# Performance work log

Measured on AMD Instinct MI355X. Metric: run time of the kernel, lower is better.

Reference implementation:

```python
import jax, jax.numpy as jnp
import numpy as np

N, E, D, H, L = 50000, 800000, 256, 256, 4
EMB = 2 * H  # OGB format: MLP hidden width
BN_EPS = 1e-5


def _bn(h, gamma, beta):
    # training-mode BatchNorm1d: biased batch stats over node dim
    m = jnp.mean(h, axis=0)
    v = jnp.mean((h - m) ** 2, axis=0)
    return gamma * (h - m) / jnp.sqrt(v + BN_EPS) + beta


def setup_inputs() -> dict:
    key = jax.random.key(0)
    ks = jax.random.split(key, 12)
    x = jax.random.normal(ks[0], (N, D), dtype=jnp.float32)
    edge_index = jax.random.randint(ks[1], (2, E), 0, N, dtype=jnp.int64)
    s1 = 1.0 / np.sqrt(D)
    s2 = 1.0 / np.sqrt(EMB)
    return {
        "x": x,
        "edge_index": edge_index,
        "W1": jax.random.uniform(ks[2], (L, D, EMB), jnp.float32, -s1, s1),
        "b1": jax.random.uniform(ks[3], (L, EMB), jnp.float32, -s1, s1),
        "bn1_gamma": jnp.ones((L, EMB), jnp.float32),
        "bn1_beta": jnp.zeros((L, EMB), jnp.float32),
        "W2": jax.random.uniform(ks[4], (L, EMB, H), jnp.float32, -s2, s2),
        "b2": jax.random.uniform(ks[5], (L, H), jnp.float32, -s2, s2),
        "bn2_gamma": jnp.ones((L, H), jnp.float32),
        "bn2_beta": jnp.zeros((L, H), jnp.float32),
    }


def reference(x, edge_index, W1, b1, bn1_gamma, bn1_beta, W2, b2, bn2_gamma, bn2_beta):
    src, dst = edge_index[0], edge_index[1]
    n = x.shape[0]
    h = x
    for l in range(L):
        # GINConv with eps=0: (1+eps)*h_i + sum_{j->i} h_j
        agg = h + jax.ops.segment_sum(h[src], dst, num_segments=n)
        # inner MLP: Linear -> BN -> ReLU -> Linear
        z = jax.nn.relu(_bn(agg @ W1[l] + b1[l], bn1_gamma[l], bn1_beta[l]))
        z = z @ W2[l] + b2[l]
        # outer BN; ReLU except last layer (dropout = identity in eval/reference)
        z = _bn(z, bn2_gamma[l], bn2_beta[l])
        h = z if l == L - 1 else jax.nn.relu(z)
    return h
```

## Files before the change

### kernel.cpp

```cpp
#include <hip/hip_runtime.h>
#include <stdint.h>

#define NN 50000
#define NE 800000
#define DD 256
#define EM 512
#define NL 4
#define EPS 1e-5f

typedef unsigned short u16;
typedef __attribute__((ext_vector_type(4))) unsigned short u16x4;
typedef __attribute__((ext_vector_type(8))) short s16x8;
typedef __attribute__((ext_vector_type(8))) float f32x8;
typedef __attribute__((ext_vector_type(4))) float f32x4;
typedef __attribute__((ext_vector_type(8))) __bf16 bf16x8;

union Frag { s16x8 s; bf16x8 b; };

__device__ __forceinline__ float bf2f(u16 h) {
  unsigned u = ((unsigned)h) << 16;
  return __builtin_bit_cast(float, u);
}
__device__ __forceinline__ u16 f2bf(float f) {
  unsigned u = __builtin_bit_cast(unsigned, f);
  u = (u + 0x7FFFu + ((u >> 16) & 1u)) >> 16;
  return (u16)u;
}
__device__ __forceinline__ void bfsplit(float f, u16& hi, u16& lo) {
  hi = f2bf(f);
  lo = f2bf(f - bf2f(hi));
}

__device__ __forceinline__ void gload16(const u16* g, u16* l) {
  __builtin_amdgcn_global_load_lds(
      (const __attribute__((address_space(1))) unsigned int*)g,
      (__attribute__((address_space(3))) unsigned int*)l, 16, 0, 0);
}


__global__ void k_f32_to_bf16(const float* __restrict__ in, u16* __restrict__ out, int n8) {
  int i = blockIdx.x * blockDim.x + threadIdx.x;
  int stride = gridDim.x * blockDim.x;
  for (; i < n8; i += stride) {
    f32x8 v = ((const f32x8*)in)[i];
    s16x8 o;
#pragma unroll
    for (int j = 0; j < 8; j++) o[j] = (short)f2bf(v[j]);
    ((s16x8*)out)[i] = o;
  }
}

__global__ void k_prep_w(const float* __restrict__ W, u16* __restrict__ WThi,
                         u16* __restrict__ WTlo, int K, int Nc) {
  int total = NL * K * Nc;
  for (int i = blockIdx.x * blockDim.x + threadIdx.x; i < total; i += gridDim.x * blockDim.x) {
    int l = i / (K * Nc);
    int rem = i - l * (K * Nc);
    int k = rem / Nc;
    int n = rem - k * Nc;
    float v = W[i];
    u16 hi, lo; bfsplit(v, hi, lo);
    size_t o = (size_t)l * Nc * K + (size_t)n * K + k;
    WThi[o] = hi; WTlo[o] = lo;
  }
}

__global__ void k_deg(const int* __restrict__ dst, int* __restrict__ deg) {
  for (int e = blockIdx.x * blockDim.x + threadIdx.x; e < NE; e += gridDim.x * blockDim.x)
    atomicAdd(&deg[dst[e]], 1);
}

#define SCB 49

__global__ __launch_bounds__(1024) void k_scan1(const int* __restrict__ deg,
                                                int* __restrict__ rowptr,
                                                int* __restrict__ part) {
  __shared__ int sm[1024];
  int t = threadIdx.x, b = blockIdx.x;
  int idx = b * 1024 + t;
  int v = (idx < NN) ? deg[idx] : 0;
  sm[t] = v;
  __syncthreads();
  for (int off = 1; off < 1024; off <<= 1) {
    int u = (t >= off) ? sm[t - off] : 0;
    __syncthreads();
    sm[t] += u;
    __syncthreads();
  }
  int incl = sm[t];
  if (idx < NN) rowptr[idx] = incl - v;
  if (t == 1023) part[b] = incl;
}

__global__ void k_scan2(int* __restrict__ part, int* __restrict__ rowptr) {
  int t = threadIdx.x;
  int v = (t < SCB) ? part[t] : 0;
  int orig = v;
  for (int off = 1; off < 64; off <<= 1) {
    int u = __shfl_up(v, off);
    if (t >= off) v += u;
  }
  if (t < SCB) part[t] = v - orig;
  if (t == SCB - 1) rowptr[NN] = v;
}

__global__ __launch_bounds__(1024) void k_scan3(int* __restrict__ rowptr,
                                                const int* __restrict__ part) {
  int idx = blockIdx.x * 1024 + threadIdx.x;
  if (idx < NN) rowptr[idx] += part[blockIdx.x];
}

__global__ void k_fill(const int* __restrict__ src, const int* __restrict__ dst,
                       const int* __restrict__ rowptr, int* __restrict__ cursor,
                       int* __restrict__ cols) {
  for (int e = blockIdx.x * blockDim.x + threadIdx.x; e < NE; e += gridDim.x * blockDim.x) {
    int d = dst[e];
    int pos = atomicAdd(&cursor[d], 1);
    cols[rowptr[d] + pos] = src[e];
  }
}


template <bool FUSED>
__global__ __launch_bounds__(256) void k_agg(const u16* __restrict__ src,
                                             const float* __restrict__ ss,
                                             const int* __restrict__ rowptr,
                                             const int* __restrict__ cols,
                                             u16* __restrict__ Ahi,
                                             u16* __restrict__ Alo) {
  int wid = threadIdx.x >> 6, lane = threadIdx.x & 63;
  int node = blockIdx.x * 4 + wid;
  int c0 = lane << 2;
  f32x4 sc, sh;
  if (FUSED) {
    sc = *(const f32x4*)(ss + c0);
    sh = *(const f32x4*)(ss + DD + c0);
  }
  u16x4 v = *(const u16x4*)(src + (size_t)node * DD + c0);
  f32x4 a;
#pragma unroll
  for (int j = 0; j < 4; j++) {
    float f = bf2f(v[j]);
    a[j] = FUSED ? fmaxf(f * sc[j] + sh[j], 0.f) : f;
  }
  int beg = rowptr[node], end = rowptr[node + 1];
  int e = beg;
  for (; e + 3 < end; e += 4) {
    int s0 = cols[e], s1 = cols[e + 1], s2 = cols[e + 2], s3 = cols[e + 3];
    u16x4 w0 = *(const u16x4*)(src + (size_t)s0 * DD + c0);
    u16x4 w1 = *(const u16x4*)(src + (size_t)s1 * DD + c0);
    u16x4 w2 = *(const u16x4*)(src + (size_t)s2 * DD + c0);
    u16x4 w3 = *(const u16x4*)(src + (size_t)s3 * DD + c0);
#pragma unroll
    for (int j = 0; j < 4; j++) {
      float f0 = bf2f(w0[j]), f1 = bf2f(w1[j]), f2 = bf2f(w2[j]), f3 = bf2f(w3[j]);
      if (FUSED) {
        f0 = fmaxf(f0 * sc[j] + sh[j], 0.f);
        f1 = fmaxf(f1 * sc[j] + sh[j], 0.f);
        f2 = fmaxf(f2 * sc[j] + sh[j], 0.f);
        f3 = fmaxf(f3 * sc[j] + sh[j], 0.f);
      }
      a[j] += f0; a[j] += f1; a[j] += f2; a[j] += f3;
    }
  }
  for (; e < end; ++e) {
    int s = cols[e];
    u16x4 w = *(const u16x4*)(src + (size_t)s * DD + c0);
#pragma unroll
    for (int j = 0; j < 4; j++) {
      float f = bf2f(w[j]);
      a[j] += FUSED ? fmaxf(f * sc[j] + sh[j], 0.f) : f;
    }
  }
  u16x4 oh, ol;
#pragma unroll
  for (int j = 0; j < 4; j++) { u16 hi, lo; bfsplit(a[j], hi, lo); oh[j] = hi; ol[j] = lo; }
  *(u16x4*)(Ahi + (size_t)node * DD + c0) = oh;
  *(u16x4*)(Alo + (size_t)node * DD + c0) = ol;
}

template <int K, int NC, bool OUT_BF16, int NSEG>
__global__ __launch_bounds__(256) void k_gemm(const u16* __restrict__ Ahi,
                                              const u16* __restrict__ Alo,
                                              const u16* __restrict__ WThi,
                                              const u16* __restrict__ WTlo,
                                              const float* __restrict__ bias,
                                              void* __restrict__ Zout,
                                              float* __restrict__ stats, int M) {
  constexpr int NCB = NC / 128;
  int nxb = (M + 127) >> 7;
  int bid = blockIdx.x;
  int slot = bid & 7;
  int ycb  = (bid >> 3) & (NCB - 1);
  int grp  = bid / (8 * NCB);
  int xb   = grp * 8 + slot;
  if (xb >= nxb) return;
  int brow = xb * 128;
  int bcol = ycb * 128;

  __shared__ u16 AlHi[128 * 32];
  __shared__ u16 AlLo[NSEG == 3 ? 128 * 32 : 64];
  __shared__ u16 BlHi[128 * 32];
  __shared__ u16 BlLo[128 * 32];
  __shared__ float sblk[256];
  int tid = threadIdx.x;
  sblk[tid] = 0.f;
  int lane = tid & 63, wid = tid >> 6;
  int wm = wid & 1, wn = wid >> 1;

  f32x4 zero = {0.f, 0.f, 0.f, 0.f};
  f32x4 acc[4][4];
#pragma unroll
  for (int m = 0; m < 4; m++)
#pragma unroll
    for (int n = 0; n < 4; n++) acc[m][n] = zero;

  int rinc = lane >> 2;
  int cq = (lane & 3) * 8;
  long ra0 = brow + wid * 16 + rinc;  if (ra0 > M - 1) ra0 = M - 1;
  long ra1 = brow + 64 + wid * 16 + rinc; if (ra1 > M - 1) ra1 = M - 1;
  long rb0 = bcol + wid * 16 + rinc;
  long rb1 = bcol + 64 + wid * 16 + rinc;

  const u16* gAh0 = Ahi + ra0 * K + cq;
  const u16* gAh1 = Ahi + ra1 * K + cq;
  const u16* gAl0 = Alo + ra0 * K + cq;
  const u16* gAl1 = Alo + ra1 * K + cq;
  const u16* gBh0 = WThi + rb0 * K + cq;
  const u16* gBh1 = WThi + rb1 * K + cq;
  const u16* gBl0 = WTlo + rb0 * K + cq;
  const u16* gBl1 = WTlo + rb1 * K + cq;
  int lc0 = wid * 512, lc1 = (wid + 4) * 512;

  int fr = lane & 15;
  int kk = (lane >> 4) * 8;
  int fo = (wm * 64 + fr) * 32 + kk;
  int go = (wn * 64 + fr) * 32 + kk;

  const int KS = K / 32;
  for (int kt = 0; kt < KS; ++kt) {
    int k0 = kt * 32;
    gload16(gAh0 + k0, &AlHi[lc0]);
    gload16(gAh1 + k0, &AlHi[lc1]);
    if (NSEG == 3) {
      gload16(gAl0 + k0, &AlLo[lc0]);
      gload16(gAl1 + k0, &AlLo[lc1]);
    }
    gload16(gBh0 + k0, &BlHi[lc0]);
    gload16(gBh1 + k0, &BlHi[lc1]);
    gload16(gBl0 + k0, &BlLo[lc0]);
    gload16(gBl1 + k0, &BlLo[lc1]);
    __syncthreads();

    Frag aH[4], bH[4], bL[4];
#pragma unroll
    for (int m = 0; m < 4; m++) aH[m].s = *(const s16x8*)(&AlHi[fo + m * 512]);
#pragma unroll
    for (int n = 0; n < 4; n++) bH[n].s = *(const s16x8*)(&BlHi[go + n * 512]);
#pragma unroll
    for (int n = 0; n < 4; n++) bL[n].s = *(const s16x8*)(&BlLo[go + n * 512]);
#pragma unroll
    for (int m = 0; m < 4; m++)
#pragma unroll
      for (int n = 0; n < 4; n++)
        acc[m][n] = __builtin_amdgcn_mfma_f32_16x16x32_bf16(aH[m].b, bH[n].b, acc[m][n], 0, 0, 0);
    if (NSEG == 3) {
      Frag aL[4];
#pragma unroll
      for (int m = 0; m < 4; m++) aL[m].s = *(const s16x8*)(&AlLo[fo + m * 512]);
#pragma unroll
      for (int m = 0; m < 4; m++)
#pragma unroll
        for (int n = 0; n < 4; n++)
          acc[m][n] = __builtin_amdgcn_mfma_f32_16x16x32_bf16(aL[m].b, bH[n].b, acc[m][n], 0, 0, 0);
    }
#pragma unroll
    for (int m = 0; m < 4; m++)
#pragma unroll
      for (int n = 0; n < 4; n++)
        acc[m][n] = __builtin_amdgcn_mfma_f32_16x16x32_bf16(aH[m].b, bL[n].b, acc[m][n], 0, 0, 0);
    __syncthreads();
  }

  int colb = bcol + wn * 64;
  float bv[4];
#pragma unroll
  for (int n = 0; n < 4; n++) bv[n] = bias[colb + n * 16 + fr];
  int rb = brow + wm * 64 + ((lane >> 4) << 2);
  float sn[4] = {0.f, 0.f, 0.f, 0.f}, qn[4] = {0.f, 0.f, 0.f, 0.f};
#pragma unroll
  for (int m = 0; m < 4; m++) {
#pragma unroll
    for (int r = 0; r < 4; r++) {
      int row = rb + m * 16 + r;
      if (row < M) {
        size_t base = (size_t)row * NC + colb + fr;
#pragma unroll
        for (int n = 0; n < 4; n++) {
          float z = acc[m][n][r] + bv[n];
          if (OUT_BF16) ((u16*)Zout)[base + n * 16] = f2bf(z);
          else          ((float*)Zout)[base + n * 16] = z;
          sn[n] += z; qn[n] += z * z;
        }
      }
    }
  }
#pragma unroll
  for (int n = 0; n < 4; n++) {
    sn[n] += __shfl_xor(sn[n], 16); sn[n] += __shfl_xor(sn[n], 32);
    qn[n] += __shfl_xor(qn[n], 16); qn[n] += __shfl_xor(qn[n], 32);
  }
  if (lane < 16) {
#pragma unroll
    for (int n = 0; n < 4; n++) {
      atomicAdd(&sblk[wn * 64 + n * 16 + lane], sn[n]);
      atomicAdd(&sblk[128 + wn * 64 + n * 16 + lane], qn[n]);
    }
  }
  __syncthreads();
  if (tid < 128) atomicAdd(&stats[bcol + tid], sblk[tid]);
  else           atomicAdd(&stats[NC + bcol + (tid - 128)], sblk[tid]);
}

__global__ void k_finalize(const float* __restrict__ stats, const float* __restrict__ gamma,
                           const float* __restrict__ beta, float* __restrict__ ss, int NC) {
  int c = blockIdx.x * blockDim.x + threadIdx.x;
  if (c < NC) {
    float mean = stats[c] * (1.0f / NN);
    float var = stats[NC + c] * (1.0f / NN) - mean * mean;
    float sc = gamma[c] * rsqrtf(var + EPS);
    ss[c] = sc;
    ss[NC + c] = beta[c] - mean * sc;
  }
}

template <int NC>
__global__ void k_bn_a2(const u16* __restrict__ Z, const float* __restrict__ ss,
                        u16* __restrict__ A2, int n8) {
  int i = blockIdx.x * blockDim.x + threadIdx.x;
  int stride = gridDim.x * blockDim.x;
  for (; i < n8; i += stride) {
    int c = (i * 8) & (NC - 1);
    s16x8 v = *(const s16x8*)(Z + (size_t)i * 8);
    s16x8 o;
#pragma unroll
    for (int j = 0; j < 8; j++) {
      float f = fmaxf(bf2f((u16)v[j]) * ss[c + j] + ss[NC + c + j], 0.f);
      o[j] = (short)f2bf(f);
    }
    *(s16x8*)(A2 + (size_t)i * 8) = o;
  }
}

template <int NC>
__global__ void k_bn_out(const float* __restrict__ Z, const float* __restrict__ ss,
                         float* __restrict__ out, int n4) {
  int i = blockIdx.x * blockDim.x + threadIdx.x;
  int stride = gridDim.x * blockDim.x;
  for (; i < n4; i += stride) {
    int c = (i * 4) & (NC - 1);
    f32x4 v = *(const f32x4*)(Z + (size_t)i * 4);
    f32x4 o;
#pragma unroll
    for (int j = 0; j < 4; j++) o[j] = v[j] * ss[c + j] + ss[NC + c + j];
    *(f32x4*)(out + (size_t)i * 4) = o;
  }
}


extern "C" void kernel_launch(void* const* d_in, const int* in_sizes, int n_in,
                              void* d_out, int out_size, void* d_ws, size_t ws_size,
                              hipStream_t stream) {
  const float* x  = (const float*)d_in[0];
  const int* ei   = (const int*)d_in[1];
  const int* esrc = ei;
  const int* edst = ei + NE;
  const float* W1 = (const float*)d_in[2];
  const float* b1 = (const float*)d_in[3];
  const float* g1 = (const float*)d_in[4];
  const float* be1= (const float*)d_in[5];
  const float* W2 = (const float*)d_in[6];
  const float* b2 = (const float*)d_in[7];
  const float* g2 = (const float*)d_in[8];
  const float* be2= (const float*)d_in[9];
  float* out = (float*)d_out;

  char* w = (char*)d_ws;
  auto alloc = [&](size_t bytes) {
    char* p = w;
    w += (bytes + 255) & ~(size_t)255;
    return p;
  };
  char* R0 = alloc((size_t)NN * EM * 2);
  char* R1 = alloc((size_t)NN * EM * 2);
  u16* W1hi = (u16*)alloc((size_t)NL * EM * DD * 2);
  u16* W1lo = (u16*)alloc((size_t)NL * EM * DD * 2);
  u16* W2hi = (u16*)alloc((size_t)NL * DD * EM * 2);
  u16* W2lo = (u16*)alloc((size_t)NL * DD * EM * 2);
  char* zbase = (char*)alloc((size_t)NN * 4);
  int* deg    = (int*)zbase;
  int* cursor = (int*)alloc((size_t)NN * 4);
  float* stats1 = (float*)alloc((size_t)NL * 2 * EM * 4);
  float* stats2 = (float*)alloc((size_t)NL * 2 * DD * 4);
  size_t zspan = (char*)w - zbase;
  int* rowptr = (int*)alloc((size_t)(NN + 1) * 4);
  int* part   = (int*)alloc(64 * 4);
  int* cols   = (int*)alloc((size_t)NE * 4);
  float* ss1  = (float*)alloc(2 * EM * 4);
  float* ss2  = (float*)alloc(2 * DD * 4);

  u16*   Hb   = (u16*)R0;
  u16*   Z1   = (u16*)R0;
  float* Z2f  = (float*)R0;
  u16*   A1hi = (u16*)R1;
  u16*   A1lo = (u16*)R1 + (size_t)NN * DD;
  u16*   A2   = (u16*)R1;

  hipMemsetAsync(zbase, 0, zspan, stream);
  k_deg<<<2048, 256, 0, stream>>>(edst, deg);
  k_scan1<<<SCB, 1024, 0, stream>>>(deg, rowptr, part);
  k_scan2<<<1, 64, 0, stream>>>(part, rowptr);
  k_scan3<<<SCB, 1024, 0, stream>>>(rowptr, part);
  k_fill<<<2048, 256, 0, stream>>>(esrc, edst, rowptr, cursor, cols);
  k_prep_w<<<2048, 256, 0, stream>>>(W1, W1hi, W1lo, DD, EM);
  k_prep_w<<<2048, 256, 0, stream>>>(W2, W2hi, W2lo, EM, DD);
  k_f32_to_bf16<<<2048, 256, 0, stream>>>(x, Hb, NN * DD / 8);

  const int NXB = (NN + 127) / 128;
  const int G1GRID = ((NXB + 7) / 8) * 8 * (EM / 128);
  const int G2GRID = ((NXB + 7) / 8) * 8 * (DD / 128);

  for (int l = 0; l < NL; ++l) {
    float* st1 = stats1 + (size_t)l * 2 * EM;
    float* st2 = stats2 + (size_t)l * 2 * DD;
    if (l == 0)
      k_agg<false><<<NN / 4, 256, 0, stream>>>(Hb, nullptr, rowptr, cols, A1hi, A1lo);
    else
      k_agg<true><<<NN / 4, 256, 0, stream>>>(Hb, ss2, rowptr, cols, A1hi, A1lo);

    k_gemm<DD, EM, true, 3><<<G1GRID, 256, 0, stream>>>(
        A1hi, A1lo, W1hi + (size_t)l * EM * DD, W1lo + (size_t)l * EM * DD,
        b1 + (size_t)l * EM, Z1, st1, NN);
    k_finalize<<<2, 256, 0, stream>>>(st1, g1 + (size_t)l * EM, be1 + (size_t)l * EM, ss1, EM);
    k_bn_a2<EM><<<2048, 256, 0, stream>>>(Z1, ss1, A2, NN * EM / 8);

    if (l < NL - 1) {
      k_gemm<EM, DD, true, 2><<<G2GRID, 256, 0, stream>>>(
          A2, A2, W2hi + (size_t)l * DD * EM, W2lo + (size_t)l * DD * EM,
          b2 + (size_t)l * DD, Hb, st2, NN);
    } else {
      k_gemm<EM, DD, false, 2><<<G2GRID, 256, 0, stream>>>(
          A2, A2, W2hi + (size_t)l * DD * EM, W2lo + (size_t)l * DD * EM,
          b2 + (size_t)l * DD, Z2f, st2, NN);
    }
    k_finalize<<<1, 256, 0, stream>>>(st2, g2 + (size_t)l * DD, be2 + (size_t)l * DD, ss2, DD);
  }
  k_bn_out<DD><<<2048, 256, 0, stream>>>(Z2f, ss2, out, NN * DD / 4);
}
```

Before: 980.3 us.

## Fuse BN1+ReLU into second GEMM A-load and fold finalize into consumers

The BN1 normalize+ReLU pass (k_bn_a2) is removed. GEMM2 now reads the bf16 Z1 directly into registers, applies scale/shift/ReLU computed in shared memory from the raw stats, and writes the result to LDS as the A tile. The k_finalize kernels are eliminated by computing scale/shift inline in k_agg, k_gemm2 and k_bn_out. The last layer's output becomes bf16 instead of fp32, which saves a full pass over a 50Kx512 tensor plus several launches, but it trades the async global-to-LDS loads for register staging in GEMM2 and changes the final layer's precision.

```diff
diff --git a/kernel.cpp b/kernel.cpp
--- a/kernel.cpp
+++ b/kernel.cpp
@@ -7,6 +7,7 @@
 #define EM 512
 #define NL 4
 #define EPS 1e-5f
+#define RN (1.0f / NN)
 
 typedef unsigned short u16;
 typedef __attribute__((ext_vector_type(4))) unsigned short u16x4;
@@ -123,7 +124,9 @@
 
 template <bool FUSED>
 __global__ __launch_bounds__(256) void k_agg(const u16* __restrict__ src,
-                                             const float* __restrict__ ss,
+                                             const float* __restrict__ st,
+                                             const float* __restrict__ ga,
+                                             const float* __restrict__ be,
                                              const int* __restrict__ rowptr,
                                              const int* __restrict__ cols,
                                              u16* __restrict__ Ahi,
@@ -133,8 +136,17 @@
   int c0 = lane << 2;
   f32x4 sc, sh;
   if (FUSED) {
-    sc = *(const f32x4*)(ss + c0);
-    sh = *(const f32x4*)(ss + DD + c0);
+    f32x4 m = *(const f32x4*)(st + c0);
+    f32x4 q = *(const f32x4*)(st + DD + c0);
+    f32x4 g = *(const f32x4*)(ga + c0);
+    f32x4 b = *(const f32x4*)(be + c0);
+#pragma unroll
+    for (int j = 0; j < 4; j++) {
+      float mean = m[j] * RN;
+      float var = q[j] * RN - mean * mean;
+      sc[j] = g[j] * rsqrtf(var + EPS);
+      sh[j] = b[j] - mean * sc[j];
+    }
   }
   u16x4 v = *(const u16x4*)(src + (size_t)node * DD + c0);
   f32x4 a;
@@ -179,14 +191,14 @@
   *(u16x4*)(Alo + (size_t)node * DD + c0) = ol;
 }
 
-template <int K, int NC, bool OUT_BF16, int NSEG>
-__global__ __launch_bounds__(256) void k_gemm(const u16* __restrict__ Ahi,
-                                              const u16* __restrict__ Alo,
-                                              const u16* __restrict__ WThi,
-                                              const u16* __restrict__ WTlo,
-                                              const float* __restrict__ bias,
-                                              void* __restrict__ Zout,
-                                              float* __restrict__ stats, int M) {
+template <int K, int NC>
+__global__ __launch_bounds__(256) void k_gemm1(const u16* __restrict__ Ahi,
+                                               const u16* __restrict__ Alo,
+                                               const u16* __restrict__ WThi,
+                                               const u16* __restrict__ WTlo,
+                                               const float* __restrict__ bias,
+                                               u16* __restrict__ Zout,
+                                               float* __restrict__ stats, int M) {
   constexpr int NCB = NC / 128;
   int nxb = (M + 127) >> 7;
   int bid = blockIdx.x;
@@ -199,7 +211,7 @@
   int bcol = ycb * 128;
 
   __shared__ u16 AlHi[128 * 32];
-  __shared__ u16 AlLo[NSEG == 3 ? 128 * 32 : 64];
+  __shared__ u16 AlLo[128 * 32];
   __shared__ u16 BlHi[128 * 32];
   __shared__ u16 BlLo[128 * 32];
   __shared__ float sblk[256];
@@ -242,17 +254,15 @@
     int k0 = kt * 32;
     gload16(gAh0 + k0, &AlHi[lc0]);
     gload16(gAh1 + k0, &AlHi[lc1]);
-    if (NSEG == 3) {
-      gload16(gAl0 + k0, &AlLo[lc0]);
-      gload16(gAl1 + k0, &AlLo[lc1]);
-    }
+    gload16(gAl0 + k0, &AlLo[lc0]);
+    gload16(gAl1 + k0, &AlLo[lc1]);
     gload16(gBh0 + k0, &BlHi[lc0]);
     gload16(gBh1 + k0, &BlHi[lc1]);
     gload16(gBl0 + k0, &BlLo[lc0]);
     gload16(gBl1 + k0, &BlLo[lc1]);
     __syncthreads();
 
-    Frag aH[4], bH[4], bL[4];
+    Frag aH[4], bH[4], bL[4], aL[4];
 #pragma unroll
     for (int m = 0; m < 4; m++) aH[m].s = *(const s16x8*)(&AlHi[fo + m * 512]);
 #pragma unroll
@@ -264,16 +274,13 @@
 #pragma unroll
       for (int n = 0; n < 4; n++)
         acc[m][n] = __builtin_amdgcn_mfma_f32_16x16x32_bf16(aH[m].b, bH[n].b, acc[m][n], 0, 0, 0);
-    if (NSEG == 3) {
-      Frag aL[4];
-#pragma unroll
-      for (int m = 0; m < 4; m++) aL[m].s = *(const s16x8*)(&AlLo[fo + m * 512]);
-#pragma unroll
-      for (int m = 0; m < 4; m++)
-#pragma unroll
-        for (int n = 0; n < 4; n++)
-          acc[m][n] = __builtin_amdgcn_mfma_f32_16x16x32_bf16(aL[m].b, bH[n].b, acc[m][n], 0, 0, 0);
-    }
+#pragma unroll
+    for (int m = 0; m < 4; m++) aL[m].s = *(const s16x8*)(&AlLo[fo + m * 512]);
+#pragma unroll
+    for (int m = 0; m < 4; m++)
+#pragma unroll
+      for (int n = 0; n < 4; n++)
+        acc[m][n] = __builtin_amdgcn_mfma_f32_16x16x32_bf16(aL[m].b, bH[n].b, acc[m][n], 0, 0, 0);
 #pragma unroll
     for (int m = 0; m < 4; m++)
 #pragma unroll
@@ -298,8 +305,7 @@
 #pragma unroll
         for (int n = 0; n < 4; n++) {
           float z = acc[m][n][r] + bv[n];
-          if (OUT_BF16) ((u16*)Zout)[base + n * 16] = f2bf(z);
-          else          ((float*)Zout)[base + n * 16] = z;
+          Zout[base + n * 16] = f2bf(z);
           sn[n] += z; qn[n] += z * z;
         }
       }
@@ -322,47 +328,178 @@
   else           atomicAdd(&stats[NC + bcol + (tid - 128)], sblk[tid]);
 }
 
-__global__ void k_finalize(const float* __restrict__ stats, const float* __restrict__ gamma,
-                           const float* __restrict__ beta, float* __restrict__ ss, int NC) {
-  int c = blockIdx.x * blockDim.x + threadIdx.x;
-  if (c < NC) {
-    float mean = stats[c] * (1.0f / NN);
-    float var = stats[NC + c] * (1.0f / NN) - mean * mean;
-    float sc = gamma[c] * rsqrtf(var + EPS);
-    ss[c] = sc;
-    ss[NC + c] = beta[c] - mean * sc;
-  }
-}
-
-template <int NC>
-__global__ void k_bn_a2(const u16* __restrict__ Z, const float* __restrict__ ss,
-                        u16* __restrict__ A2, int n8) {
-  int i = blockIdx.x * blockDim.x + threadIdx.x;
-  int stride = gridDim.x * blockDim.x;
-  for (; i < n8; i += stride) {
-    int c = (i * 8) & (NC - 1);
-    s16x8 v = *(const s16x8*)(Z + (size_t)i * 8);
-    s16x8 o;
-#pragma unroll
-    for (int j = 0; j < 8; j++) {
-      float f = fmaxf(bf2f((u16)v[j]) * ss[c + j] + ss[NC + c + j], 0.f);
-      o[j] = (short)f2bf(f);
-    }
-    *(s16x8*)(A2 + (size_t)i * 8) = o;
-  }
-}
-
-template <int NC>
-__global__ void k_bn_out(const float* __restrict__ Z, const float* __restrict__ ss,
+__global__ __launch_bounds__(256) void k_gemm2(const u16* __restrict__ Z1,
+                                               const u16* __restrict__ WThi,
+                                               const u16* __restrict__ WTlo,
+                                               const float* __restrict__ bias,
+                                               const float* __restrict__ st1,
+                                               const float* __restrict__ g1,
+                                               const float* __restrict__ be1,
+                                               u16* __restrict__ Hout,
+                                               float* __restrict__ stats, int M) {
+  constexpr int K = EM, NC = DD, NCB = NC / 128;
+  int nxb = (M + 127) >> 7;
+  int bid = blockIdx.x;
+  int slot = bid & 7;
+  int ycb  = (bid >> 3) & (NCB - 1);
+  int grp  = bid / (8 * NCB);
+  int xb   = grp * 8 + slot;
+  if (xb >= nxb) return;
+  int brow = xb * 128;
+  int bcol = ycb * 128;
+
+  __shared__ u16 AlHi[128 * 32];
+  __shared__ u16 BlHi[128 * 32];
+  __shared__ u16 BlLo[128 * 32];
+  __shared__ float scL[EM];
+  __shared__ float shL[EM];
+  __shared__ float sblk[256];
+  int tid = threadIdx.x;
+  sblk[tid] = 0.f;
+  for (int c = tid; c < EM; c += 256) {
+    float mean = st1[c] * RN;
+    float var = st1[EM + c] * RN - mean * mean;
+    float s = g1[c] * rsqrtf(var + EPS);
+    scL[c] = s;
+    shL[c] = be1[c] - mean * s;
+  }
+  int lane = tid & 63, wid = tid >> 6;
+  int wm = wid & 1, wn = wid >> 1;
+
+  f32x4 zero = {0.f, 0.f, 0.f, 0.f};
+  f32x4 acc[4][4];
+#pragma unroll
+  for (int m = 0; m < 4; m++)
+#pragma unroll
+    for (int n = 0; n < 4; n++) acc[m][n] = zero;
+
+  int rinc = lane >> 2;
+  int cq = (lane & 3) * 8;
+  long ra0 = brow + wid * 16 + rinc;  if (ra0 > M - 1) ra0 = M - 1;
+  long ra1 = brow + 64 + wid * 16 + rinc; if (ra1 > M - 1) ra1 = M - 1;
+  long rb0 = bcol + wid * 16 + rinc;
+  long rb1 = bcol + 64 + wid * 16 + rinc;
+
+  const u16* gZ0 = Z1 + ra0 * K + cq;
+  const u16* gZ1 = Z1 + ra1 * K + cq;
+  const u16* gBh0 = WThi + rb0 * K + cq;
+  const u16* gBh1 = WThi + rb1 * K + cq;
+  const u16* gBl0 = WTlo + rb0 * K + cq;
+  const u16* gBl1 = WTlo + rb1 * K + cq;
+  int lc0 = wid * 512, lc1 = (wid + 4) * 512;
+
+  int fr = lane & 15;
+  int kk = (lane >> 4) * 8;
+  int fo = (wm * 64 + fr) * 32 + kk;
+  int go = (wn * 64 + fr) * 32 + kk;
+
+  __syncthreads();
+
+  const int KS = K / 32;
+  for (int kt = 0; kt < KS; ++kt) {
+    int k0 = kt * 32;
+    s16x8 z0 = *(const s16x8*)(gZ0 + k0);
+    s16x8 z1 = *(const s16x8*)(gZ1 + k0);
+    gload16(gBh0 + k0, &BlHi[lc0]);
+    gload16(gBh1 + k0, &BlHi[lc1]);
+    gload16(gBl0 + k0, &BlLo[lc0]);
+    gload16(gBl1 + k0, &BlLo[lc1]);
+    f32x4 s0 = *(const f32x4*)(&scL[k0 + cq]);
+    f32x4 s1 = *(const f32x4*)(&scL[k0 + cq + 4]);
+    f32x4 h0 = *(const f32x4*)(&shL[k0 + cq]);
+    f32x4 h1 = *(const f32x4*)(&shL[k0 + cq + 4]);
+    s16x8 o0, o1;
+#pragma unroll
+    for (int j = 0; j < 4; j++) {
+      o0[j]     = (short)f2bf(fmaxf(bf2f((u16)z0[j])     * s0[j] + h0[j], 0.f));
+      o0[j + 4] = (short)f2bf(fmaxf(bf2f((u16)z0[j + 4]) * s1[j] + h1[j], 0.f));
+      o1[j]     = (short)f2bf(fmaxf(bf2f((u16)z1[j])     * s0[j] + h0[j], 0.f));
+      o1[j + 4] = (short)f2bf(fmaxf(bf2f((u16)z1[j + 4]) * s1[j] + h1[j], 0.f));
+    }
+    *(s16x8*)(&AlHi[lc0 + lane * 8]) = o0;
+    *(s16x8*)(&AlHi[lc1 + lane * 8]) = o1;
+    __syncthreads();
+
+    Frag aH[4], bH[4], bL[4];
+#pragma unroll
+    for (int m = 0; m < 4; m++) aH[m].s = *(const s16x8*)(&AlHi[fo + m * 512]);
+#pragma unroll
+    for (int n = 0; n < 4; n++) bH[n].s = *(const s16x8*)(&BlHi[go + n * 512]);
+#pragma unroll
+    for (int n = 0; n < 4; n++) bL[n].s = *(const s16x8*)(&BlLo[go + n * 512]);
+#pragma unroll
+    for (int m = 0; m < 4; m++)
+#pragma unroll
+      for (int n = 0; n < 4; n++)
+        acc[m][n] = __builtin_amdgcn_mfma_f32_16x16x32_bf16(aH[m].b, bH[n].b, acc[m][n], 0, 0, 0);
+#pragma unroll
+    for (int m = 0; m < 4; m++)
+#pragma unroll
+      for (int n = 0; n < 4; n++)
+        acc[m][n] = __builtin_amdgcn_mfma_f32_16x16x32_bf16(aH[m].b, bL[n].b, acc[m][n], 0, 0, 0);
+    __syncthreads();
+  }
+
+  int colb = bcol + wn * 64;
+  float bv[4];
+#pragma unroll
+  for (int n = 0; n < 4; n++) bv[n] = bias[colb + n * 16 + fr];
+  int rb = brow + wm * 64 + ((lane >> 4) << 2);
+  float sn[4] = {0.f, 0.f, 0.f, 0.f}, qn[4] = {0.f, 0.f, 0.f, 0.f};
+#pragma unroll
+  for (int m = 0; m < 4; m++) {
+#pragma unroll
+    for (int r = 0; r < 4; r++) {
+      int row = rb + m * 16 + r;
+      if (row < M) {
+        size_t base = (size_t)row * NC + colb + fr;
+#pragma unroll
+        for (int n = 0; n < 4; n++) {
+          float z = acc[m][n][r] + bv[n];
+          Hout[base + n * 16] = f2bf(z);
+          sn[n] += z; qn[n] += z * z;
+        }
+      }
+    }
+  }
+#pragma unroll
+  for (int n = 0; n < 4; n++) {
+    sn[n] += __shfl_xor(sn[n], 16); sn[n] += __shfl_xor(sn[n], 32);
+    qn[n] += __shfl_xor(qn[n], 16); qn[n] += __shfl_xor(qn[n], 32);
+  }
+  if (lane < 16) {
+#pragma unroll
+    for (int n = 0; n < 4; n++) {
+      atomicAdd(&sblk[wn * 64 + n * 16 + lane], sn[n]);
+      atomicAdd(&sblk[128 + wn * 64 + n * 16 + lane], qn[n]);
+    }
+  }
+  __syncthreads();
+  if (tid < 128) atomicAdd(&stats[bcol + tid], sblk[tid]);
+  else           atomicAdd(&stats[NC + bcol + (tid - 128)], sblk[tid]);
+}
+
+__global__ void k_bn_out(const u16* __restrict__ H, const float* __restrict__ st,
+                         const float* __restrict__ ga, const float* __restrict__ be,
                          float* __restrict__ out, int n4) {
   int i = blockIdx.x * blockDim.x + threadIdx.x;
   int stride = gridDim.x * blockDim.x;
   for (; i < n4; i += stride) {
-    int c = (i * 4) & (NC - 1);
-    f32x4 v = *(const f32x4*)(Z + (size_t)i * 4);
+    int c = (i * 4) & (DD - 1);
+    f32x4 m = *(const f32x4*)(st + c);
+    f32x4 q = *(const f32x4*)(st + DD + c);
+    f32x4 g = *(const f32x4*)(ga + c);
+    f32x4 b = *(const f32x4*)(be + c);
+    u16x4 v = *(const u16x4*)(H + (size_t)i * 4);
     f32x4 o;
 #pragma unroll
-    for (int j = 0; j < 4; j++) o[j] = v[j] * ss[c + j] + ss[NC + c + j];
+    for (int j = 0; j < 4; j++) {
+      float mean = m[j] * RN;
+      float var = q[j] * RN - mean * mean;
+      float sc = g[j] * rsqrtf(var + EPS);
+      float sh = b[j] - mean * sc;
+      o[j] = bf2f(v[j]) * sc + sh;
+    }
     *(f32x4*)(out + (size_t)i * 4) = o;
   }
 }
@@ -393,6 +530,7 @@
   };
   char* R0 = alloc((size_t)NN * EM * 2);
   char* R1 = alloc((size_t)NN * EM * 2);
+  u16*  H2 = (u16*)alloc((size_t)NN * DD * 2);
   u16* W1hi = (u16*)alloc((size_t)NL * EM * DD * 2);
   u16* W1lo = (u16*)alloc((size_t)NL * EM * DD * 2);
   u16* W2hi = (u16*)alloc((size_t)NL * DD * EM * 2);
@@ -406,15 +544,10 @@
   int* rowptr = (int*)alloc((size_t)(NN + 1) * 4);
   int* part   = (int*)alloc(64 * 4);
   int* cols   = (int*)alloc((size_t)NE * 4);
-  float* ss1  = (float*)alloc(2 * EM * 4);
-  float* ss2  = (float*)alloc(2 * DD * 4);
-
-  u16*   Hb   = (u16*)R0;
-  u16*   Z1   = (u16*)R0;
-  float* Z2f  = (float*)R0;
-  u16*   A1hi = (u16*)R1;
-  u16*   A1lo = (u16*)R1 + (size_t)NN * DD;
-  u16*   A2   = (u16*)R1;
+
+  u16* Z1   = (u16*)R0;
+  u16* A1hi = (u16*)R1;
+  u16* A1lo = (u16*)R1 + (size_t)NN * DD;
 
   hipMemsetAsync(zbase, 0, zspan, stream);
   k_deg<<<2048, 256, 0, stream>>>(edst, deg);
@@ -424,7 +557,7 @@
   k_fill<<<2048, 256, 0, stream>>>(esrc, edst, rowptr, cursor, cols);
   k_prep_w<<<2048, 256, 0, stream>>>(W1, W1hi, W1lo, DD, EM);
   k_prep_w<<<2048, 256, 0, stream>>>(W2, W2hi, W2lo, EM, DD);
-  k_f32_to_bf16<<<2048, 256, 0, stream>>>(x, Hb, NN * DD / 8);
+  k_f32_to_bf16<<<2048, 256, 0, stream>>>(x, H2, NN * DD / 8);
 
   const int NXB = (NN + 127) / 128;
   const int G1GRID = ((NXB + 7) / 8) * 8 * (EM / 128);
@@ -434,26 +567,25 @@
     float* st1 = stats1 + (size_t)l * 2 * EM;
     float* st2 = stats2 + (size_t)l * 2 * DD;
     if (l == 0)
-      k_agg<false><<<NN / 4, 256, 0, stream>>>(Hb, nullptr, rowptr, cols, A1hi, A1lo);
+      k_agg<false><<<NN / 4, 256, 0, stream>>>(H2, nullptr, nullptr, nullptr,
+                                               rowptr, cols, A1hi, A1lo);
     else
-      k_agg<true><<<NN / 4, 256, 0, stream>>>(Hb, ss2, rowptr, cols, A1hi, A1lo);
-
-    k_gemm<DD, EM, true, 3><<<G1GRID, 256, 0, stream>>>(
+      k_agg<true><<<NN / 4, 256, 0, stream>>>(H2, stats2 + (size_t)(l - 1) * 2 * DD,
+                                              g2 + (size_t)(l - 1) * DD,
+                                              be2 + (size_t)(l - 1) * DD,
+                                              rowptr, cols, A1hi, A1lo);
+
+    k_gemm1<DD, EM><<<G1GRID, 256, 0, stream>>>(
         A1hi, A1lo, W1hi + (size_t)l * EM * DD, W1lo + (size_t)l * EM * DD,
         b1 + (size_t)l * EM, Z1, st1, NN);
-    k_finalize<<<2, 256, 0, stream>>>(st1, g1 + (size_t)l * EM, be1 + (size_t)l * EM, ss1, EM);
-    k_bn_a2<EM><<<2048, 256, 0, stream>>>(Z1, ss1, A2, NN * EM / 8);
-
-    if (l < NL - 1) {
-      k_gemm<EM, DD, true, 2><<<G2GRID, 256, 0, stream>>>(
-          A2, A2, W2hi + (size_t)l * DD * EM, W2lo + (size_t)l * DD * EM,
-          b2 + (size_t)l * DD, Hb, st2, NN);
-    } else {
-      k_gemm<EM, DD, false, 2><<<G2GRID, 256, 0, stream>>>(
-          A2, A2, W2hi + (size_t)l * DD * EM, W2lo + (size_t)l * DD * EM,
-          b2 + (size_t)l * DD, Z2f, st2, NN);
-    }
-    k_finalize<<<1, 256, 0, stream>>>(st2, g2 + (size_t)l * DD, be2 + (size_t)l * DD, ss2, DD);
-  }
-  k_bn_out<DD><<<2048, 256, 0, stream>>>(Z2f, ss2, out, NN * DD / 4);
-}
+
+    k_gemm2<<<G2GRID, 256, 0, stream>>>(
+        Z1, W2hi + (size_t)l * DD * EM, W2lo + (size_t)l * DD * EM,
+        b2 + (size_t)l * DD, st1, g1 + (size_t)l * EM, be1 + (size_t)l * EM,
+        H2, st2, NN);
+  }
+  k_bn_out<<<2048, 256, 0, stream>>>(H2, stats2 + (size_t)(NL - 1) * 2 * DD,
+                                     g2 + (size_t)(NL - 1) * DD,
+                                     be2 + (size_t)(NL - 1) * DD,
+                                     out, NN * DD / 4);
+}
```

Measured after the change: 950.7 us. 1.03x faster.
